# Kernel tuning notes

Hardware: AMD Instinct MI355X
Metric: run time of the kernel (lower is better)

Reference implementation:

```python
import jax, jax.numpy as jnp
import numpy as np

N_NODES = 100000
N_REL = 5
IN_F = 128
HID = 128

def _glorot(key, shape):
    fan_in, fan_out = shape[-2], shape[-1]
    s = jnp.sqrt(6.0 / (fan_in + fan_out))
    return jax.random.uniform(key, shape, jnp.float32, -s, s)

def setup_inputs() -> dict:
    key = jax.random.key(0)
    ks = jax.random.split(key, 16)
    x = jax.random.normal(ks[0], (N_NODES, IN_F), jnp.float32)
    edge_index = jax.random.randint(ks[1], (2, 1600000), 0, N_NODES, jnp.int32)
    edge_type = jax.random.randint(ks[2], (1600000,), 0, N_REL, jnp.int32)
    d = {"x": x, "edge_index": edge_index, "edge_type": edge_type}
    dims = [(IN_F, HID), (HID, HID), (HID, HID)]
    for li, (fi, fo) in enumerate(dims, start=1):
        d[f"W{li}"] = _glorot(ks[3 * li], (N_REL, fi, fo))        # per-relation weights
        d[f"root{li}"] = _glorot(ks[3 * li + 1], (fi, fo))        # root/self weight
        d[f"b{li}"] = jnp.zeros((fo,), jnp.float32)               # bias
    return d

def _rgcn_conv(x, src, dst, edge_type, W, root, b):
    # out = x @ root + b + sum_r segment_mean_r(x[src] @ W_r -> dst)
    out = x @ root + b
    for r in range(N_REL):  # small fixed relation count
        m = (edge_type == r).astype(x.dtype)                      # [E]
        h = (x @ W[r])[src] * m[:, None]                          # [E, out]
        s = jax.ops.segment_sum(h, dst, num_segments=N_NODES)     # [N, out]
        c = jax.ops.segment_sum(m, dst, num_segments=N_NODES)     # [N]
        out = out + s / jnp.maximum(c, 1.0)[:, None]
    return out

def reference(x, edge_index, edge_type, W1, root1, b1, W2, root2, b2, W3, root3, b3):
    src, dst = edge_index[0], edge_index[1]
    # dropout is identity in eval mode; applied as identity here
    h = jax.nn.relu(_rgcn_conv(x, src, dst, edge_type, W1, root1, b1))
    h = jax.nn.relu(_rgcn_conv(h, src, dst, edge_type, W2, root2, b2))
    h = jax.nn.relu(_rgcn_conv(h, src, dst, edge_type, W3, root3, b3))
    return h
```

## Files before the change

kernel.cpp:

```cpp
#include <hip/hip_runtime.h>

#define N_NODES_C 100000
#define N_REL_C 5
#define N_TOT (N_REL_C * N_NODES_C)
#define FEAT 128
#define KTOT 768
#define BM 128
#define GBK 64
#define NSWEEP 4

typedef __attribute__((ext_vector_type(8))) short bf16x8;
typedef __attribute__((ext_vector_type(4))) float f32x4;

__device__ inline unsigned short f2bf(float f) {
    union { float f; unsigned int u; } v; v.f = f;
    return (unsigned short)((v.u + 0x7FFFu + ((v.u >> 16) & 1u)) >> 16);
}

__device__ __forceinline__ unsigned int cvt_pk_bf16(float lo, float hi) {
    unsigned int r;
    asm("v_cvt_pk_bf16_f32 %0, %1, %2" : "=v"(r) : "v"(lo), "v"(hi));
    return r;
}

__device__ __forceinline__ void g2l16(const void* g, void* l) {
    __builtin_amdgcn_global_load_lds((const __attribute__((address_space(1))) unsigned int*)g,
                                     (__attribute__((address_space(3))) unsigned int*)l,
                                     16, 0, 0);
}

__device__ __forceinline__ void acc8(float (&a)[8], uint4 u) {
    union { unsigned int u; float f; } t;
    t.u = u.x << 16;         a[0] += t.f;
    t.u = u.x & 0xFFFF0000u; a[1] += t.f;
    t.u = u.y << 16;         a[2] += t.f;
    t.u = u.y & 0xFFFF0000u; a[3] += t.f;
    t.u = u.z << 16;         a[4] += t.f;
    t.u = u.z & 0xFFFF0000u; a[5] += t.f;
    t.u = u.w << 16;         a[6] += t.f;
    t.u = u.w & 0xFFFF0000u; a[7] += t.f;
}

__global__ __launch_bounds__(256) void count_edges(const int* __restrict__ dst,
                                                   const int* __restrict__ et,
                                                   int* __restrict__ cnt, int E) {
    int e = blockIdx.x * 256 + threadIdx.x;
    if (e < E) atomicAdd(&cnt[et[e] * N_NODES_C + dst[e]], 1);
}

__global__ __launch_bounds__(256) void make_inv(const int* __restrict__ cnt,
                                                float* __restrict__ inv, int n) {
    int i = blockIdx.x * 256 + threadIdx.x;
    if (i < n) inv[i] = 1.0f / (float)(cnt[i] > 1 ? cnt[i] : 1);
}

__global__ __launch_bounds__(256) void scan_block(const int* __restrict__ cnt,
                                                  int* __restrict__ rowptr,
                                                  int* __restrict__ bsum, int n) {
    __shared__ int sh[256];
    int tid = threadIdx.x;
    int i = blockIdx.x * 256 + tid;
    int v = (i < n) ? cnt[i] : 0;
    sh[tid] = v;
    __syncthreads();
#pragma unroll
    for (int o = 1; o < 256; o <<= 1) {
        int t = (tid >= o) ? sh[tid - o] : 0;
        __syncthreads();
        sh[tid] += t;
        __syncthreads();
    }
    if (i < n) rowptr[i] = sh[tid] - v;
    if (tid == 255) bsum[blockIdx.x] = sh[255];
}

__global__ __launch_bounds__(256) void scan_bsum(int* __restrict__ bsum, int nb) {
    __shared__ int sh[256];
    __shared__ int carry;
    int tid = threadIdx.x;
    if (tid == 0) carry = 0;
    __syncthreads();
    for (int base = 0; base < nb; base += 256) {
        int i = base + tid;
        int v = (i < nb) ? bsum[i] : 0;
        sh[tid] = v;
        __syncthreads();
#pragma unroll
        for (int o = 1; o < 256; o <<= 1) {
            int t = (tid >= o) ? sh[tid - o] : 0;
            __syncthreads();
            sh[tid] += t;
            __syncthreads();
        }
        int excl = sh[tid] - v + carry;
        int chunk_total = sh[255];
        __syncthreads();
        if (i < nb) bsum[i] = excl;
        if (tid == 0) carry += chunk_total;
        __syncthreads();
    }
}

__global__ __launch_bounds__(256) void scan_add(int* __restrict__ rowptr,
                                                const int* __restrict__ bsum,
                                                int n, int Etot) {
    int i = blockIdx.x * 256 + threadIdx.x;
    if (i < n) rowptr[i] += bsum[blockIdx.x];
    if (i == 0) rowptr[n] = Etot;
}

__global__ __launch_bounds__(256) void fill_csr_sweep(const int* __restrict__ src,
                                                      const int* __restrict__ dst,
                                                      const int* __restrict__ et,
                                                      int* __restrict__ cursor,
                                                      int* __restrict__ esrc,
                                                      int E, int klo, int khi) {
    int e = blockIdx.x * 256 + threadIdx.x;
    if (e < E) {
        int key = et[e] * N_NODES_C + dst[e];
        if ((unsigned)(key - klo) < (unsigned)(khi - klo)) {
            int pos = atomicAdd(&cursor[key], 1);
            esrc[pos] = src[e];
        }
    }
}

__global__ __launch_bounds__(256) void convert_x(const float* __restrict__ x,
                                                 unsigned short* __restrict__ xb, int n4) {
    int i = blockIdx.x * 256 + threadIdx.x;
    if (i >= n4) return;
    float4 v = ((const float4*)x)[i];
    ushort4 o;
    o.x = f2bf(v.x); o.y = f2bf(v.y); o.z = f2bf(v.z); o.w = f2bf(v.w);
    ((ushort4*)xb)[i] = o;
}

__global__ __launch_bounds__(256) void convert_w(const float* __restrict__ root,
                                                 const float* __restrict__ W,
                                                 unsigned short* __restrict__ Bt) {
    int idx = blockIdx.x * 256 + threadIdx.x;
    if (idx >= FEAT * KTOT) return;
    int c = idx / KTOT;
    int kv = idx - c * KTOT;
    float val;
    if (kv < FEAT) {
        val = root[kv * FEAT + c];
    } else {
        int r = (kv - FEAT) >> 7;
        int kk = (kv - FEAT) & 127;
        val = W[((size_t)r * FEAT + kk) * FEAT + c];
    }
    Bt[idx] = f2bf(val);
}

__global__ __launch_bounds__(256) void gather_mean(const unsigned short* __restrict__ hb,
                                                   const int* __restrict__ esrc,
                                                   const int* __restrict__ rowptr,
                                                   const float* __restrict__ inv,
                                                   unsigned short* __restrict__ agg,
                                                   int chunk0, int CL) {
    int qw = threadIdx.x >> 4;
    int seg = threadIdx.x & 15;
    int local = blockIdx.x * 16 + qw;
    if (local >= CL) return;
    int r = blockIdx.y;
    int node = chunk0 + local;
    int lo = rowptr[r * N_NODES_C + node];
    int hi = rowptr[r * N_NODES_C + node + 1];

    float a0[8], a1[8];
#pragma unroll
    for (int j = 0; j < 8; j++) { a0[j] = 0.f; a1[j] = 0.f; }

    const unsigned short* hseg = hb + seg * 8;

    int e = lo;
    for (; e + 4 <= hi; e += 4) {
        int s0 = esrc[e];
        int s1 = esrc[e + 1];
        int s2 = esrc[e + 2];
        int s3 = esrc[e + 3];
        uint4 u0 = *(const uint4*)(hseg + ((size_t)s0 << 7));
        uint4 u1 = *(const uint4*)(hseg + ((size_t)s1 << 7));
        uint4 u2 = *(const uint4*)(hseg + ((size_t)s2 << 7));
        uint4 u3 = *(const uint4*)(hseg + ((size_t)s3 << 7));
        acc8(a0, u0);
        acc8(a1, u1);
        acc8(a0, u2);
        acc8(a1, u3);
    }
    if (e + 2 <= hi) {
        int s0 = esrc[e];
        int s1 = esrc[e + 1];
        uint4 u0 = *(const uint4*)(hseg + ((size_t)s0 << 7));
        uint4 u1 = *(const uint4*)(hseg + ((size_t)s1 << 7));
        acc8(a0, u0);
        acc8(a1, u1);
        e += 2;
    }
    if (e < hi) {
        int s = esrc[e];
        uint4 u = *(const uint4*)(hseg + ((size_t)s << 7));
        acc8(a0, u);
    }

    float sc = inv[r * N_NODES_C + node];
    uint4 o;
    o.x = cvt_pk_bf16((a0[0] + a1[0]) * sc, (a0[1] + a1[1]) * sc);
    o.y = cvt_pk_bf16((a0[2] + a1[2]) * sc, (a0[3] + a1[3]) * sc);
    o.z = cvt_pk_bf16((a0[4] + a1[4]) * sc, (a0[5] + a1[5]) * sc);
    o.w = cvt_pk_bf16((a0[6] + a1[6]) * sc, (a0[7] + a1[7]) * sc);
    *(uint4*)(agg + (((size_t)r * CL + local) << 7) + seg * 8) = o;
}

__global__ __launch_bounds__(256) void rgcn_gemm(const unsigned short* __restrict__ hb,
                                                 const unsigned short* __restrict__ agg,
                                                 const unsigned short* __restrict__ Bt,
                                                 const float* __restrict__ bias,
                                                 float* __restrict__ outf,
                                                 unsigned short* __restrict__ outb,
                                                 int chunk0, int CL) {
    __shared__ unsigned short As[BM * GBK];
    __shared__ unsigned short Bs[FEAT * GBK];

    const int tid = threadIdx.x;
    const int w = tid >> 6, lane = tid & 63;
    const int wr = w >> 1, wc = w & 1;
    const int lm = lane & 15, lq = lane >> 4;
    const int brow0 = blockIdx.x * BM;

    f32x4 acc[4][4];
#pragma unroll
    for (int i = 0; i < 4; i++)
#pragma unroll
        for (int j = 0; j < 4; j++) acc[i][j] = (f32x4){0.f, 0.f, 0.f, 0.f};

    size_t hboff[4];
    size_t aggoff[4];
    size_t boff[4];
    int ldsbase[4];
#pragma unroll
    for (int i = 0; i < 4; i++) {
        int cid = (w * 4 + i) * 64 + lane;
        int row = cid >> 3;
        int cs = (cid & 7) ^ (row & 7);
        int gr = brow0 + row;
        if (gr >= CL) gr = CL - 1;
        hboff[i]  = ((size_t)(chunk0 + gr) << 7) + cs * 8;
        aggoff[i] = ((size_t)gr << 7) + cs * 8;
        boff[i]   = (size_t)row * KTOT + cs * 8;
        ldsbase[i] = ((w * 4 + i) * 64) * 8;
    }

    for (int kb = 0; kb < KTOT; kb += GBK) {
        __syncthreads();
        if (kb < FEAT) {
#pragma unroll
            for (int i = 0; i < 4; i++)
                g2l16(hb + hboff[i] + kb, &As[ldsbase[i]]);
        } else {
            size_t reloff = (((size_t)((kb - FEAT) >> 7)) * CL << 7) + (size_t)((kb - FEAT) & 127);
#pragma unroll
            for (int i = 0; i < 4; i++)
                g2l16(agg + aggoff[i] + reloff, &As[ldsbase[i]]);
        }
#pragma unroll
        for (int i = 0; i < 4; i++)
            g2l16(Bt + boff[i] + kb, &Bs[ldsbase[i]]);
        __syncthreads();

#pragma unroll
        for (int h = 0; h < 2; h++) {
            bf16x8 af[4], bf[4];
#pragma unroll
            for (int t = 0; t < 4; t++) {
                int row = wr * 64 + t * 16 + lm;
                int ca = (h * 4 + lq) ^ (row & 7);
                af[t] = *(const bf16x8*)&As[row * GBK + ca * 8];
                int col = wc * 64 + t * 16 + lm;
                int cb = (h * 4 + lq) ^ (col & 7);
                bf[t] = *(const bf16x8*)&Bs[col * GBK + cb * 8];
            }
#pragma unroll
            for (int i = 0; i < 4; i++)
#pragma unroll
                for (int j = 0; j < 4; j++)
                    acc[i][j] = __builtin_amdgcn_mfma_f32_16x16x32_bf16(af[i], bf[j], acc[i][j], 0, 0, 0);
        }
    }

    float bcol[4];
#pragma unroll
    for (int j = 0; j < 4; j++) bcol[j] = bias[wc * 64 + j * 16 + lm];

#pragma unroll
    for (int i = 0; i < 4; i++) {
#pragma unroll
        for (int reg = 0; reg < 4; reg++) {
            int lr = brow0 + wr * 64 + i * 16 + lq * 4 + reg;
            if (lr < CL) {
                size_t grow = (size_t)(chunk0 + lr) << 7;
#pragma unroll
                for (int j = 0; j < 4; j++) {
                    float v = acc[i][j][reg] + bcol[j];
                    v = fmaxf(v, 0.f);
                    int col = wc * 64 + j * 16 + lm;
                    if (outf) outf[grow + col] = v;
                    else outb[grow + col] = f2bf(v);
                }
            }
        }
    }
}

extern "C" void kernel_launch(void* const* d_in, const int* in_sizes, int n_in,
                              void* d_out, int out_size, void* d_ws, size_t ws_size,
                              hipStream_t stream) {
    const float* x = (const float*)d_in[0];
    const int* ei  = (const int*)d_in[1];
    const int* et  = (const int*)d_in[2];
    const int E = in_sizes[2];
    const int* src  = ei;
    const int* dstp = ei + E;

    int CL = 25000;
    if (ws_size >= 61997056ull + 100000ull * 1280ull + 589824ull) CL = 100000;
    else if (ws_size >= 61997056ull + 50000ull * 1280ull + 589824ull) CL = 50000;
    const int NCHUNK = N_NODES_C / CL;

    char* ws = (char*)d_ws;
    float* inv             = (float*)ws;
    int*   rowptr          = (int*)(ws + 2097152);
    int*   esrc            = (int*)(ws + 4194304);
    unsigned short* xbA    = (unsigned short*)(ws + 10616832);
    unsigned short* xbB    = (unsigned short*)(ws + 36306944);
    unsigned short* agg    = (unsigned short*)(ws + 61997056);
    unsigned short* BtAll  = (unsigned short*)(ws + 61997056 + (size_t)CL * 1280ull);
    int*   cnt    = (int*)(ws + 61997056);
    int*   cursor = (int*)(ws + 61997056 + 2097152);
    int*   bsum   = (int*)(ws + 61997056 + 4194304);

    const int nscan_blocks = (N_TOT + 255) / 256;

    hipMemsetAsync(cnt, 0, (size_t)N_TOT * 4, stream);
    count_edges<<<(E + 255) / 256, 256, 0, stream>>>(dstp, et, cnt, E);
    make_inv<<<(N_TOT + 255) / 256, 256, 0, stream>>>(cnt, inv, N_TOT);
    scan_block<<<nscan_blocks, 256, 0, stream>>>(cnt, rowptr, bsum, N_TOT);
    scan_bsum<<<1, 256, 0, stream>>>(bsum, nscan_blocks);
    scan_add<<<nscan_blocks, 256, 0, stream>>>(rowptr, bsum, N_TOT, E);
    hipMemcpyAsync(cursor, rowptr, (size_t)N_TOT * 4, hipMemcpyDeviceToDevice, stream);
    {
        const int kspan = N_TOT / NSWEEP;
        for (int s = 0; s < NSWEEP; s++)
            fill_csr_sweep<<<(E + 255) / 256, 256, 0, stream>>>(src, dstp, et, cursor,
                                                                esrc, E, s * kspan,
                                                                (s + 1) * kspan);
    }

    const int n4 = N_NODES_C * FEAT / 4;
    convert_x<<<(n4 + 255) / 256, 256, 0, stream>>>(x, xbA, n4);

    const float* Wp[3] = {(const float*)d_in[3], (const float*)d_in[6], (const float*)d_in[9]};
    const float* Rp[3] = {(const float*)d_in[4], (const float*)d_in[7], (const float*)d_in[10]};
    const float* Bp[3] = {(const float*)d_in[5], (const float*)d_in[8], (const float*)d_in[11]};

    const int nw = FEAT * KTOT;
    for (int l = 0; l < 3; l++)
        convert_w<<<(nw + 255) / 256, 256, 0, stream>>>(Rp[l], Wp[l],
                                                        BtAll + (size_t)l * nw);

    const int gemm_grid = (CL + BM - 1) / BM;
    dim3 ggrid((CL + 15) / 16, N_REL_C);

    for (int l = 0; l < 3; l++) {
        const unsigned short* hin = (l == 1) ? xbB : xbA;
        unsigned short* outb = (l == 0) ? xbB : ((l == 1) ? xbA : nullptr);
        float* outf = (l == 2) ? (float*)d_out : nullptr;
        for (int c = 0; c < NCHUNK; c++) {
            gather_mean<<<ggrid, 256, 0, stream>>>(hin, esrc, rowptr, inv, agg,
                                                   c * CL, CL);
            rgcn_gemm<<<gemm_grid, 256, 0, stream>>>(hin, agg, BtAll + (size_t)l * nw,
                                                     Bp[l], outf, outb, c * CL, CL);
        }
    }
}
```

Baseline: 662.3 us.

## Fuse per-relation gather-mean into the GEMM via shared-memory aggregation tiles

```diff
diff --git a/kernel.cpp b/kernel.cpp
--- a/kernel.cpp
+++ b/kernel.cpp
@@ -153,80 +153,22 @@
     Bt[idx] = f2bf(val);
 }
 
-__global__ __launch_bounds__(256) void gather_mean(const unsigned short* __restrict__ hb,
-                                                   const int* __restrict__ esrc,
-                                                   const int* __restrict__ rowptr,
-                                                   const float* __restrict__ inv,
-                                                   unsigned short* __restrict__ agg,
-                                                   int chunk0, int CL) {
-    int qw = threadIdx.x >> 4;
-    int seg = threadIdx.x & 15;
-    int local = blockIdx.x * 16 + qw;
-    if (local >= CL) return;
-    int r = blockIdx.y;
-    int node = chunk0 + local;
-    int lo = rowptr[r * N_NODES_C + node];
-    int hi = rowptr[r * N_NODES_C + node + 1];
-
-    float a0[8], a1[8];
-#pragma unroll
-    for (int j = 0; j < 8; j++) { a0[j] = 0.f; a1[j] = 0.f; }
-
-    const unsigned short* hseg = hb + seg * 8;
-
-    int e = lo;
-    for (; e + 4 <= hi; e += 4) {
-        int s0 = esrc[e];
-        int s1 = esrc[e + 1];
-        int s2 = esrc[e + 2];
-        int s3 = esrc[e + 3];
-        uint4 u0 = *(const uint4*)(hseg + ((size_t)s0 << 7));
-        uint4 u1 = *(const uint4*)(hseg + ((size_t)s1 << 7));
-        uint4 u2 = *(const uint4*)(hseg + ((size_t)s2 << 7));
-        uint4 u3 = *(const uint4*)(hseg + ((size_t)s3 << 7));
-        acc8(a0, u0);
-        acc8(a1, u1);
-        acc8(a0, u2);
-        acc8(a1, u3);
-    }
-    if (e + 2 <= hi) {
-        int s0 = esrc[e];
-        int s1 = esrc[e + 1];
-        uint4 u0 = *(const uint4*)(hseg + ((size_t)s0 << 7));
-        uint4 u1 = *(const uint4*)(hseg + ((size_t)s1 << 7));
-        acc8(a0, u0);
-        acc8(a1, u1);
-        e += 2;
-    }
-    if (e < hi) {
-        int s = esrc[e];
-        uint4 u = *(const uint4*)(hseg + ((size_t)s << 7));
-        acc8(a0, u);
-    }
-
-    float sc = inv[r * N_NODES_C + node];
-    uint4 o;
-    o.x = cvt_pk_bf16((a0[0] + a1[0]) * sc, (a0[1] + a1[1]) * sc);
-    o.y = cvt_pk_bf16((a0[2] + a1[2]) * sc, (a0[3] + a1[3]) * sc);
-    o.z = cvt_pk_bf16((a0[4] + a1[4]) * sc, (a0[5] + a1[5]) * sc);
-    o.w = cvt_pk_bf16((a0[6] + a1[6]) * sc, (a0[7] + a1[7]) * sc);
-    *(uint4*)(agg + (((size_t)r * CL + local) << 7) + seg * 8) = o;
-}
-
-__global__ __launch_bounds__(256) void rgcn_gemm(const unsigned short* __restrict__ hb,
-                                                 const unsigned short* __restrict__ agg,
-                                                 const unsigned short* __restrict__ Bt,
-                                                 const float* __restrict__ bias,
-                                                 float* __restrict__ outf,
-                                                 unsigned short* __restrict__ outb,
-                                                 int chunk0, int CL) {
-    __shared__ unsigned short As[BM * GBK];
-    __shared__ unsigned short Bs[FEAT * GBK];
+__global__ __launch_bounds__(256, 3) void rgcn_fused(const unsigned short* __restrict__ hb,
+                                                     const unsigned short* __restrict__ Bt,
+                                                     const int* __restrict__ esrc,
+                                                     const int* __restrict__ rowptr,
+                                                     const float* __restrict__ inv,
+                                                     const float* __restrict__ bias,
+                                                     float* __restrict__ outf,
+                                                     unsigned short* __restrict__ outb) {
+    __shared__ __align__(16) unsigned short Ap[BM * FEAT];
+    __shared__ __align__(16) unsigned short Bs[FEAT * GBK];
 
     const int tid = threadIdx.x;
     const int w = tid >> 6, lane = tid & 63;
     const int wr = w >> 1, wc = w & 1;
     const int lm = lane & 15, lq = lane >> 4;
+    const int qw = tid >> 4, seg = tid & 15;
     const int brow0 = blockIdx.x * BM;
 
     f32x4 acc[4][4];
@@ -236,7 +178,6 @@
         for (int j = 0; j < 4; j++) acc[i][j] = (f32x4){0.f, 0.f, 0.f, 0.f};
 
     size_t hboff[4];
-    size_t aggoff[4];
     size_t boff[4];
     int ldsbase[4];
 #pragma unroll
@@ -245,25 +186,17 @@
         int row = cid >> 3;
         int cs = (cid & 7) ^ (row & 7);
         int gr = brow0 + row;
-        if (gr >= CL) gr = CL - 1;
-        hboff[i]  = ((size_t)(chunk0 + gr) << 7) + cs * 8;
-        aggoff[i] = ((size_t)gr << 7) + cs * 8;
-        boff[i]   = (size_t)row * KTOT + cs * 8;
+        if (gr >= N_NODES_C) gr = N_NODES_C - 1;
+        hboff[i] = ((size_t)gr << 7) + cs * 8;
+        boff[i]  = (size_t)row * KTOT + cs * 8;
         ldsbase[i] = ((w * 4 + i) * 64) * 8;
     }
 
-    for (int kb = 0; kb < KTOT; kb += GBK) {
-        __syncthreads();
-        if (kb < FEAT) {
-#pragma unroll
-            for (int i = 0; i < 4; i++)
-                g2l16(hb + hboff[i] + kb, &As[ldsbase[i]]);
-        } else {
-            size_t reloff = (((size_t)((kb - FEAT) >> 7)) * CL << 7) + (size_t)((kb - FEAT) & 127);
-#pragma unroll
-            for (int i = 0; i < 4; i++)
-                g2l16(agg + aggoff[i] + reloff, &As[ldsbase[i]]);
-        }
+    for (int kb = 0; kb < FEAT; kb += GBK) {
+        __syncthreads();
+#pragma unroll
+        for (int i = 0; i < 4; i++)
+            g2l16(hb + hboff[i] + kb, &Ap[ldsbase[i]]);
 #pragma unroll
         for (int i = 0; i < 4; i++)
             g2l16(Bt + boff[i] + kb, &Bs[ldsbase[i]]);
@@ -276,7 +209,7 @@
             for (int t = 0; t < 4; t++) {
                 int row = wr * 64 + t * 16 + lm;
                 int ca = (h * 4 + lq) ^ (row & 7);
-                af[t] = *(const bf16x8*)&As[row * GBK + ca * 8];
+                af[t] = *(const bf16x8*)&Ap[row * GBK + ca * 8];
                 int col = wc * 64 + t * 16 + lm;
                 int cb = (h * 4 + lq) ^ (col & 7);
                 bf[t] = *(const bf16x8*)&Bs[col * GBK + cb * 8];
@@ -289,6 +222,81 @@
         }
     }
 
+    for (int r = 0; r < N_REL_C; r++) {
+        const int kb0 = FEAT + r * FEAT;
+        __syncthreads();
+#pragma unroll
+        for (int i = 0; i < 4; i++)
+            g2l16(Bt + boff[i] + kb0, &Bs[ldsbase[i]]);
+
+        for (int j = 0; j < 8; j++) {
+            int n = j * 16 + qw;
+            int node = brow0 + n;
+            if (node < N_NODES_C) {
+                int idx = r * N_NODES_C + node;
+                int lo = rowptr[idx];
+                int hi = rowptr[idx + 1];
+                float a0[8], a1[8];
+#pragma unroll
+                for (int k = 0; k < 8; k++) { a0[k] = 0.f; a1[k] = 0.f; }
+                const unsigned short* hseg = hb + seg * 8;
+                int e = lo;
+                for (; e + 2 <= hi; e += 2) {
+                    int s0 = esrc[e];
+                    int s1 = esrc[e + 1];
+                    uint4 u0 = *(const uint4*)(hseg + ((size_t)s0 << 7));
+                    uint4 u1 = *(const uint4*)(hseg + ((size_t)s1 << 7));
+                    acc8(a0, u0);
+                    acc8(a1, u1);
+                }
+                if (e < hi) {
+                    int s = esrc[e];
+                    uint4 u = *(const uint4*)(hseg + ((size_t)s << 7));
+                    acc8(a0, u);
+                }
+                float sc = inv[idx];
+                uint4 o;
+                o.x = cvt_pk_bf16((a0[0] + a1[0]) * sc, (a0[1] + a1[1]) * sc);
+                o.y = cvt_pk_bf16((a0[2] + a1[2]) * sc, (a0[3] + a1[3]) * sc);
+                o.z = cvt_pk_bf16((a0[4] + a1[4]) * sc, (a0[5] + a1[5]) * sc);
+                o.w = cvt_pk_bf16((a0[6] + a1[6]) * sc, (a0[7] + a1[7]) * sc);
+                int ws = seg ^ (n & 15);
+                *(uint4*)&Ap[n * FEAT + ws * 8] = o;
+            }
+        }
+        __syncthreads();
+
+#pragma unroll
+        for (int kt = 0; kt < 2; kt++) {
+            if (kt == 1) {
+                __syncthreads();
+#pragma unroll
+                for (int i = 0; i < 4; i++)
+                    g2l16(Bt + boff[i] + kb0 + GBK, &Bs[ldsbase[i]]);
+                __syncthreads();
+            }
+#pragma unroll
+            for (int h = 0; h < 2; h++) {
+                bf16x8 af[4], bf[4];
+#pragma unroll
+                for (int t = 0; t < 4; t++) {
+                    int row = wr * 64 + t * 16 + lm;
+                    int cc = kt * 8 + h * 4 + lq;
+                    int cs2 = cc ^ (row & 15);
+                    af[t] = *(const bf16x8*)&Ap[row * FEAT + cs2 * 8];
+                    int col = wc * 64 + t * 16 + lm;
+                    int cb = (h * 4 + lq) ^ (col & 7);
+                    bf[t] = *(const bf16x8*)&Bs[col * GBK + cb * 8];
+                }
+#pragma unroll
+                for (int i = 0; i < 4; i++)
+#pragma unroll
+                    for (int j = 0; j < 4; j++)
+                        acc[i][j] = __builtin_amdgcn_mfma_f32_16x16x32_bf16(af[i], bf[j], acc[i][j], 0, 0, 0);
+            }
+        }
+    }
+
     float bcol[4];
 #pragma unroll
     for (int j = 0; j < 4; j++) bcol[j] = bias[wc * 64 + j * 16 + lm];
@@ -298,8 +306,8 @@
 #pragma unroll
         for (int reg = 0; reg < 4; reg++) {
             int lr = brow0 + wr * 64 + i * 16 + lq * 4 + reg;
-            if (lr < CL) {
-                size_t grow = (size_t)(chunk0 + lr) << 7;
+            if (lr < N_NODES_C) {
+                size_t grow = (size_t)lr << 7;
 #pragma unroll
                 for (int j = 0; j < 4; j++) {
                     float v = acc[i][j][reg] + bcol[j];
@@ -323,22 +331,16 @@
     const int* src  = ei;
     const int* dstp = ei + E;
 
-    int CL = 25000;
-    if (ws_size >= 61997056ull + 100000ull * 1280ull + 589824ull) CL = 100000;
-    else if (ws_size >= 61997056ull + 50000ull * 1280ull + 589824ull) CL = 50000;
-    const int NCHUNK = N_NODES_C / CL;
-
     char* ws = (char*)d_ws;
     float* inv             = (float*)ws;
     int*   rowptr          = (int*)(ws + 2097152);
     int*   esrc            = (int*)(ws + 4194304);
     unsigned short* xbA    = (unsigned short*)(ws + 10616832);
     unsigned short* xbB    = (unsigned short*)(ws + 36306944);
-    unsigned short* agg    = (unsigned short*)(ws + 61997056);
-    unsigned short* BtAll  = (unsigned short*)(ws + 61997056 + (size_t)CL * 1280ull);
     int*   cnt    = (int*)(ws + 61997056);
     int*   cursor = (int*)(ws + 61997056 + 2097152);
     int*   bsum   = (int*)(ws + 61997056 + 4194304);
+    unsigned short* BtAll  = (unsigned short*)(ws + 70000000);
 
     const int nscan_blocks = (N_TOT + 255) / 256;
 
@@ -369,18 +371,13 @@
         convert_w<<<(nw + 255) / 256, 256, 0, stream>>>(Rp[l], Wp[l],
                                                         BtAll + (size_t)l * nw);
 
-    const int gemm_grid = (CL + BM - 1) / BM;
-    dim3 ggrid((CL + 15) / 16, N_REL_C);
+    const int grid = (N_NODES_C + BM - 1) / BM;
 
     for (int l = 0; l < 3; l++) {
         const unsigned short* hin = (l == 1) ? xbB : xbA;
         unsigned short* outb = (l == 0) ? xbB : ((l == 1) ? xbA : nullptr);
         float* outf = (l == 2) ? (float*)d_out : nullptr;
-        for (int c = 0; c < NCHUNK; c++) {
-            gather_mean<<<ggrid, 256, 0, stream>>>(hin, esrc, rowptr, inv, agg,
-                                                   c * CL, CL);
-            rgcn_gemm<<<gemm_grid, 256, 0, stream>>>(hin, agg, BtAll + (size_t)l * nw,
-                                                     Bp[l], outf, outb, c * CL, CL);
-        }
-    }
-}
+        rgcn_fused<<<grid, 256, 0, stream>>>(hin, BtAll + (size_t)l * nw, esrc,
+                                             rowptr, inv, Bp[l], outf, outb);
+    }
+}
```

New measurement: 1.049 ms. +58.4%, slower.
